# Kernel tuning notes

Hardware: AMD Instinct MI355X
Metric: run time of the kernel (lower is better)

The kernel has to match this reference:

```python
import jax, jax.numpy as jnp
import numpy as np

NUM_POINTS = 1_000_000
WINDOW = 8                      # 2^3 corner stencil for linear shape functions in 3D
GRID = (128, 128, 128)
NUM_CELLS = GRID[0] * GRID[1] * GRID[2]
CELL = 1.0 / 64.0
INV_CELL = 64.0
ORIGIN = jnp.zeros((3,), dtype=jnp.float32)
# forward_window: the 8 corner offsets of the enclosing cell
FWD_WINDOW = jnp.array([[i, j, k] for i in (0, 1) for j in (0, 1) for k in (0, 1)],
                       dtype=jnp.int32)  # [8,3]


def setup_inputs() -> dict:
    key = jax.random.key(0)
    k1, k2, k3 = jax.random.split(key, 3)
    domain = GRID[0] * CELL
    # keep particles one cell away from the boundary so all stencil hashes are in range
    pos = jax.random.uniform(k1, (NUM_POINTS, 3), dtype=jnp.float32) * (domain - 2 * CELL) + CELL
    vel = jax.random.normal(k2, (NUM_POINTS, 3), dtype=jnp.float32)
    mass = jax.random.uniform(k3, (NUM_POINTS,), dtype=jnp.float32) * 1e-3 + 1e-4
    return {"position_stack": pos, "velocity_stack": vel, "mass_stack": mass}


def reference(position_stack, velocity_stack, mass_stack):
    # ---- get_interactions: gather particle pos, hash into grid, shape functions ----
    rel = (position_stack - ORIGIN) * INV_CELL               # [N,3] position in cell units
    base = jnp.floor(rel)                                    # [N,3]
    grid_pos = base[:, None, :] + FWD_WINDOW[None, :, :].astype(rel.dtype)  # [N,8,3]
    dist = rel[:, None, :] - grid_pos                        # [N,8,3], each dim in (-1,1)

    gp = grid_pos.astype(jnp.int32)
    # get_hash, dim==3: pos[2] + pos[0]*grid[2] + pos[1]*grid[2]*grid[0]
    intr_hash = gp[..., 2] + gp[..., 0] * GRID[2] + gp[..., 1] * (GRID[2] * GRID[0])  # [N,8]

    # linear shape function: N = prod_d (1 - |x_d|); grad scaled by inv_cell_size
    w = 1.0 - jnp.abs(dist)                                  # [N,8,3]
    shapef = w[..., 0] * w[..., 1] * w[..., 2]               # [N,8]
    valid = (intr_hash >= 0) & (intr_hash < NUM_CELLS)
    shapef = jnp.where(valid, shapef, 0.0)

    g0 = -jnp.sign(dist[..., 0]) * w[..., 1] * w[..., 2]
    g1 = -jnp.sign(dist[..., 1]) * w[..., 0] * w[..., 2]
    g2 = -jnp.sign(dist[..., 2]) * w[..., 0] * w[..., 1]
    shapef_grad = jnp.stack([g0, g1, g2], axis=-1) * INV_CELL  # [N,8,3]
    shapef_grad = jnp.where(valid[..., None], shapef_grad, 0.0)

    # intr_dist_padded = -dist * cell_size (kept implicitly via dist; used in APIC-style p2g)
    # ---- p2g scatter (vmap_intr_scatter semantics): mass & momentum to grid nodes ----
    h_flat = jnp.clip(intr_hash, 0, NUM_CELLS - 1).reshape(-1)  # [N*8]
    sm = shapef * mass_stack[:, None]                           # [N,8]
    node_mass = jax.ops.segment_sum(sm.reshape(-1), h_flat, num_segments=NUM_CELLS)   # [C]
    mom = sm[..., None] * velocity_stack[:, None, :]            # [N,8,3]
    node_mom = jax.ops.segment_sum(mom.reshape(-1, 3), h_flat, num_segments=NUM_CELLS)  # [C,3]

    return jnp.concatenate([node_mass[:, None], node_mom], axis=1)  # [C,4]
```

## Files before the change

### kernel.cpp

```cpp
#include <hip/hip_runtime.h>
#include <hip/hip_fp16.h>


#define GRID_DIM   128
#define NUM_CELLS  (GRID_DIM * GRID_DIM * GRID_DIM)
#define INV_CELL   64.0f
#define OVF_MAX    65536
#define SCAN_BLKS  2048

#define NREG       512
#define RCAP       2560
#define PPB        2048
#define MAXCAP     3
#define NT2        512
#define NSEG       125
#define NREC       2369
#define EPAD(sc)   ((sc) * 3 + ((sc) >> 2))

typedef float floatx4 __attribute__((ext_vector_type(4)));

__device__ __forceinline__ int cell_id(int ix, int iy, int iz) {
    return iz + ix * GRID_DIM + iy * (GRID_DIM * GRID_DIM);
}

__device__ __forceinline__ unsigned int q16(float f) {
    int q = (int)(f * 65536.0f + 0.5f);
    return (unsigned int)min(q, 65535);
}
__device__ __forceinline__ unsigned int f2h(float f) {
    return (unsigned int)__half_as_ushort(__float2half(f));
}
__device__ __forceinline__ float h2f(unsigned int b) {
    return __half2float(__ushort_as_half((unsigned short)(b & 0xffffu)));
}

__global__ __launch_bounds__(1024) void region_bin_kernel(
    const float* __restrict__ pos, const float* __restrict__ vel,
    const float* __restrict__ mass, unsigned int* __restrict__ region_cursor,
    uint4* __restrict__ regbuf, int* __restrict__ ovf_cnt,
    uint4* __restrict__ ovf_rec, unsigned int* __restrict__ ovf_reg, int n)
{
    __shared__ uint4 rec_lds[PPB];
    __shared__ unsigned short regof[PPB];
    __shared__ unsigned int cnt[NREG];
    __shared__ unsigned int lofs[NREG];
    __shared__ unsigned int gbase[NREG];
    __shared__ unsigned int wtot[8];

    int tid = threadIdx.x;
    int base_i = blockIdx.x * PPB;
    int blockn = min(PPB, n - base_i);

    if (tid < NREG) cnt[tid] = 0;
    __syncthreads();

    uint4 r_[2]; int reg_[2], rank_[2], val_[2];
    #pragma unroll
    for (int k = 0; k < 2; ++k) {
        int e = k * 1024 + tid;
        int i = base_i + e;
        val_[k] = (e < blockn);
        reg_[k] = 0; rank_[k] = 0;
        if (val_[k]) {
            float px = __builtin_nontemporal_load(&pos[3 * i + 0]);
            float py = __builtin_nontemporal_load(&pos[3 * i + 1]);
            float pz = __builtin_nontemporal_load(&pos[3 * i + 2]);
            float rx = px * INV_CELL, ry = py * INV_CELL, rz = pz * INV_CELL;
            float bx = floorf(rx), by = floorf(ry), bz = floorf(rz);
            float fx = rx - bx, fy = ry - by, fz = rz - bz;
            int ix = min(max((int)bx, 0), GRID_DIM - 1);
            int iy = min(max((int)by, 0), GRID_DIM - 1);
            int iz = min(max((int)bz, 0), GRID_DIM - 1);
            int reg = (iz >> 4) | ((ix >> 4) << 3) | ((iy >> 4) << 6);
            unsigned int cid = (unsigned int)((iz & 15) | ((ix & 15) << 4)
                                                        | ((iy & 15) << 8));
            float m  = __builtin_nontemporal_load(&mass[i]);
            float vx = __builtin_nontemporal_load(&vel[3 * i + 0]);
            float vy = __builtin_nontemporal_load(&vel[3 * i + 1]);
            float vz = __builtin_nontemporal_load(&vel[3 * i + 2]);
            uint4 r;
            r.x = q16(fx) | (q16(fy) << 16);
            r.y = q16(fz) | (f2h(m) << 16);
            r.z = f2h(vx) | (f2h(vy) << 16);
            r.w = f2h(vz) | (cid << 16);
            r_[k] = r;
            reg_[k] = reg;
            rank_[k] = (int)atomicAdd(&cnt[reg], 1u);
        }
    }
    __syncthreads();

    unsigned int c = 0, v = 0;
    if (tid < NREG) {
        c = cnt[tid];
        v = c;
        #pragma unroll
        for (int d = 1; d < 64; d <<= 1) {
            unsigned int t = __shfl_up(v, d, 64);
            if ((tid & 63) >= d) v += t;
        }
        if ((tid & 63) == 63) wtot[tid >> 6] = v;
    }
    __syncthreads();
    if (tid == 0) {
        unsigned int run = 0;
        #pragma unroll
        for (int w = 0; w < 8; ++w) { unsigned int t = wtot[w]; wtot[w] = run; run += t; }
    }
    __syncthreads();
    if (tid < NREG) {
        lofs[tid] = wtot[tid >> 6] + v - c;
        if (c) gbase[tid] = atomicAdd(&region_cursor[tid], c);
    }
    __syncthreads();

    #pragma unroll
    for (int k = 0; k < 2; ++k) {
        if (val_[k]) {
            int d = (int)lofs[reg_[k]] + rank_[k];
            rec_lds[d] = r_[k];
            regof[d] = (unsigned short)reg_[k];
        }
    }
    __syncthreads();

    for (int e = tid; e < blockn; e += 1024) {
        uint4 rr = rec_lds[e];
        int rg = (int)regof[e];
        unsigned int slot = gbase[rg] + (unsigned int)(e - (int)lofs[rg]);
        if (slot < (unsigned int)RCAP) {
            regbuf[(size_t)rg * RCAP + slot] = rr;
        } else {
            int o = atomicAdd(ovf_cnt, 1);
            if (o < OVF_MAX) { ovf_rec[o] = rr; ovf_reg[o] = (unsigned int)rg; }
        }
    }
}

__global__ __launch_bounds__(1024) void tile_sort_kernel(
    uint4* __restrict__ regbuf, const unsigned int* __restrict__ region_cursor,
    unsigned int* __restrict__ tile_off)
{
    __shared__ uint4 out_lds[RCAP];
    __shared__ unsigned int cnt[NT2];
    __shared__ unsigned int wsum[8];

    int r = blockIdx.x;
    int tid = threadIdx.x;
    int cntR = (int)min(region_cursor[r], (unsigned int)RCAP);

    if (tid < NT2) cnt[tid] = 0;
    __syncthreads();

    uint4 rr_[3]; int t_[3], rk_[3], vl_[3];
    #pragma unroll
    for (int k = 0; k < 3; ++k) {
        int e = k * 1024 + tid;
        vl_[k] = (e < cntR);
        t_[k] = 0; rk_[k] = 0;
        if (vl_[k]) {
            uint4 rr = regbuf[(size_t)r * RCAP + e];
            unsigned int cid = rr.w >> 16;
            int t = (int)(((cid & 15u) >> 1) | ((((cid >> 4) & 15u) >> 1) << 3)
                                             | ((((cid >> 8) & 15u) >> 1) << 6));
            rr_[k] = rr;
            t_[k] = t;
            rk_[k] = (int)atomicAdd(&cnt[t], 1u);
        }
    }
    __syncthreads();

    unsigned int c = 0, v = 0;
    if (tid < NT2) {
        c = cnt[tid];
        v = c;
        #pragma unroll
        for (int d = 1; d < 64; d <<= 1) {
            unsigned int t = __shfl_up(v, d, 64);
            if ((tid & 63) >= d) v += t;
        }
        if ((tid & 63) == 63) wsum[tid >> 6] = v;
    }
    __syncthreads();
    if (tid == 0) {
        unsigned int run = 0;
        #pragma unroll
        for (int w = 0; w < 8; ++w) { unsigned int t = wsum[w]; wsum[w] = run; run += t; }
    }
    __syncthreads();
    if (tid < NT2) cnt[tid] = wsum[tid >> 6] + v - c;
    __syncthreads();

    #pragma unroll
    for (int k = 0; k < 3; ++k)
        if (vl_[k]) out_lds[(int)cnt[t_[k]] + rk_[k]] = rr_[k];
    __syncthreads();

    for (int e = tid; e < cntR; e += 1024)
        regbuf[(size_t)r * RCAP + e] = out_lds[e];
    if (tid < NT2) tile_off[(size_t)r * (NT2 + 1) + tid] = cnt[tid];
    if (tid == 0) tile_off[(size_t)r * (NT2 + 1) + NT2] = (unsigned int)cntR;
}

__global__ __launch_bounds__(512) void tile_gather2_kernel(
    const uint4* __restrict__ regbuf, const unsigned int* __restrict__ tile_off,
    float4* __restrict__ out)
{
    __shared__ float4 recA[NREC];
    __shared__ unsigned int recB[NREC];
    __shared__ unsigned int cnt_s[729];
    __shared__ unsigned int seg_gb[NSEG];
    __shared__ unsigned short seg_reg[NSEG];
    __shared__ unsigned int seg_off[NSEG + 1];
    __shared__ unsigned int wt2[2];
    __shared__ int ovf_n;
    __shared__ short ovf_sc[64];
    __shared__ uint4 ovf_rec[64];

    int tid = threadIdx.x;
    int swz = (blockIdx.x & 7) * 512 + (blockIdx.x >> 3);
    int bz = swz & 15;
    int bx = (swz >> 4) & 15;
    int by = swz >> 8;
    int g0x = bx * 8, g0y = by * 8, g0z = bz * 8;
    int Tz0 = bz * 4 - 1, Tx0 = bx * 4 - 1, Ty0 = by * 4 - 1;

    for (int s2 = tid; s2 < 729; s2 += 512) cnt_s[s2] = 0;
    if (tid == 0) ovf_n = 0;

    unsigned int c = 0, v = 0;
    if (tid < 128) {
        if (tid < NSEG) {
            int ltz = tid % 5, q = tid / 5, ltx = q % 5, lty = q / 5;
            int Tz = Tz0 + ltz, Tx = Tx0 + ltx, Ty = Ty0 + lty;
            unsigned int gb = 0; int reg = 0;
            if ((Tz >= 0) & (Tx >= 0) & (Ty >= 0)) {
                reg = (Tz >> 3) | ((Tx >> 3) << 3) | ((Ty >> 3) << 6);
                int tl = (Tz & 7) | ((Tx & 7) << 3) | ((Ty & 7) << 6);
                unsigned int o0 = tile_off[(size_t)reg * (NT2 + 1) + tl];
                unsigned int o1 = tile_off[(size_t)reg * (NT2 + 1) + tl + 1];
                c = o1 - o0;
                gb = (unsigned int)reg * RCAP + o0;
            }
            seg_reg[tid] = (unsigned short)reg;
            seg_gb[tid] = gb;
        }
        v = c;
        #pragma unroll
        for (int d = 1; d < 64; d <<= 1) {
            unsigned int t = __shfl_up(v, d, 64);
            if ((tid & 63) >= d) v += t;
        }
        if ((tid & 63) == 63) wt2[tid >> 6] = v;
    }
    __syncthreads();
    if (tid < 128) {
        unsigned int base = (tid >= 64) ? wt2[0] : 0u;
        if (tid < NSEG) seg_off[tid] = base + v - c;
        if (tid == NSEG - 1) seg_off[NSEG] = base + v;
    }
    __syncthreads();
    int R = (int)seg_off[NSEG];

    for (int r = tid; r < R; r += 512) {
        int s = 0;
        #pragma unroll
        for (int step = 64; step >= 1; step >>= 1)
            if (s + step <= NSEG && (int)seg_off[s + step] <= r) s += step;
        int j = r - (int)seg_off[s];
        uint4 rec = regbuf[seg_gb[s] + j];
        unsigned int cid = rec.w >> 16;
        int reg = (int)seg_reg[s];
        int cz = (reg & 7) * 16 + (int)(cid & 15u);
        int cx = ((reg >> 3) & 7) * 16 + (int)((cid >> 4) & 15u);
        int cy = ((reg >> 6) & 7) * 16 + (int)((cid >> 8) & 15u);
        int uz = cz - (g0z - 1), ux = cx - (g0x - 1), uy = cy - (g0y - 1);
        if (((unsigned)uz < 9u) & ((unsigned)ux < 9u) & ((unsigned)uy < 9u)) {
            int sc = uy * 81 + ux * 9 + uz;
            unsigned int j2 = atomicAdd(&cnt_s[sc], 1u);
            if (j2 < MAXCAP) {
                int e = EPAD(sc) + (int)j2;
                float fx = (float)(rec.x & 0xffffu) * (1.0f / 65536.0f);
                float fy = (float)(rec.x >> 16)     * (1.0f / 65536.0f);
                float fz = (float)(rec.y & 0xffffu) * (1.0f / 65536.0f);
                recA[e] = make_float4(fx, fy, fz, __uint_as_float(rec.z));
                recB[e] = (rec.y >> 16) | (rec.w << 16);
            } else {
                int o = atomicAdd(&ovf_n, 1);
                if (o < 64) { ovf_sc[o] = (short)sc; ovf_rec[o] = rec; }
            }
        }
    }
    __syncthreads();

    int tz = tid & 7, tx = (tid >> 3) & 7, ty = tid >> 6;
    float a0 = 0.0f, a1 = 0.0f, a2 = 0.0f, a3 = 0.0f;

    #pragma unroll
    for (int dy = 0; dy < 2; ++dy) {
        #pragma unroll
        for (int dx = 0; dx < 2; ++dx) {
            int scb = (ty + dy) * 81 + (tx + dx) * 9 + tz;
            #pragma unroll
            for (int dz = 0; dz < 2; ++dz) {
                int sc = scb + dz;
                int cnt = min((int)cnt_s[sc], MAXCAP);
                int eb = EPAD(sc);
                for (int j = 0; j < cnt; ++j) {
                    float4 A = recA[eb + j];
                    unsigned int B = recB[eb + j];
                    unsigned int w3 = __float_as_uint(A.w);
                    float wx = dx ? (1.0f - A.x) : A.x;
                    float wy = dy ? (1.0f - A.y) : A.y;
                    float wz = dz ? (1.0f - A.z) : A.z;
                    float sm = wx * wy * wz * h2f(B);
                    a0 += sm;
                    a1 += sm * h2f(w3);
                    a2 += sm * h2f(w3 >> 16);
                    a3 += sm * h2f(B >> 16);
                }
            }
        }
    }

    int no = min(ovf_n, 64);
    for (int e2 = 0; e2 < no; ++e2) {
        int sc = (int)ovf_sc[e2];
        int uzv = sc % 9, t2 = sc / 9, uxv = t2 % 9, uyv = t2 / 9;
        int ddz = uzv - tz, ddx = uxv - tx, ddy = uyv - ty;
        if (((unsigned)ddz < 2u) & ((unsigned)ddx < 2u) & ((unsigned)ddy < 2u)) {
            uint4 rec = ovf_rec[e2];
            float fx = (float)(rec.x & 0xffffu) * (1.0f / 65536.0f);
            float fy = (float)(rec.x >> 16)     * (1.0f / 65536.0f);
            float fz = (float)(rec.y & 0xffffu) * (1.0f / 65536.0f);
            float wx = ddx ? (1.0f - fx) : fx;
            float wy = ddy ? (1.0f - fy) : fy;
            float wz = ddz ? (1.0f - fz) : fz;
            float sm = wx * wy * wz * h2f(rec.y >> 16);
            a0 += sm;
            a1 += sm * h2f(rec.z);
            a2 += sm * h2f(rec.z >> 16);
            a3 += sm * h2f(rec.w);
        }
    }

    int id = (g0z + tz) + (g0x + tx) * GRID_DIM
           + (g0y + ty) * (GRID_DIM * GRID_DIM);
    floatx4 vv = { a0, a1, a2, a3 };
    __builtin_nontemporal_store(vv, (floatx4*)&out[id]);
}

__global__ __launch_bounds__(256) void fixup_packed_kernel(
    const int* __restrict__ ovf_cnt, const uint4* __restrict__ ovf_rec,
    const unsigned int* __restrict__ ovf_reg, float* __restrict__ out)
{
    int total = min(*ovf_cnt, OVF_MAX);
    for (int k = blockIdx.x * 256 + threadIdx.x; k < total; k += gridDim.x * 256) {
        uint4 rec = ovf_rec[k];
        unsigned int reg = ovf_reg[k];
        unsigned int cid = (rec.w >> 16) & 4095u;
        int iz = (int)(reg & 7u) * 16 + (int)(cid & 15u);
        int ix = (int)((reg >> 3) & 7u) * 16 + (int)((cid >> 4) & 15u);
        int iy = (int)((reg >> 6) & 7u) * 16 + (int)((cid >> 8) & 15u);
        float fx = (float)(rec.x & 0xffffu) * (1.0f / 65536.0f);
        float fy = (float)(rec.x >> 16)     * (1.0f / 65536.0f);
        float fz = (float)(rec.y & 0xffffu) * (1.0f / 65536.0f);
        float m  = h2f(rec.y >> 16);
        float vx = h2f(rec.z), vy = h2f(rec.z >> 16), vz = h2f(rec.w);
        float wx[2] = { 1.0f - fx, fx }, wy[2] = { 1.0f - fy, fy }, wz[2] = { 1.0f - fz, fz };
        #pragma unroll
        for (int a = 0; a < 2; ++a)
            #pragma unroll
            for (int b = 0; b < 2; ++b)
                #pragma unroll
                for (int c = 0; c < 2; ++c) {
                    int h = cell_id(ix + a, iy + b, iz + c);
                    bool valid = (h >= 0) && (h < NUM_CELLS);
                    int hc = min(max(h, 0), NUM_CELLS - 1);
                    float s = valid ? (wx[a] * wy[b] * wz[c]) : 0.0f;
                    float sm = s * m;
                    float* cell = out + 4 * (size_t)hc;
                    atomicAdd(cell + 0, sm);
                    atomicAdd(cell + 1, sm * vx);
                    atomicAdd(cell + 2, sm * vy);
                    atomicAdd(cell + 3, sm * vz);
                }
    }
}

__global__ __launch_bounds__(256) void s_hist_kernel(
    const float* __restrict__ pos, int* __restrict__ counts, int n)
{
    int i = blockIdx.x * 256 + threadIdx.x;
    if (i >= n) return;
    int ix = min(max((int)floorf(pos[3 * i + 0] * INV_CELL), 0), GRID_DIM - 1);
    int iy = min(max((int)floorf(pos[3 * i + 1] * INV_CELL), 0), GRID_DIM - 1);
    int iz = min(max((int)floorf(pos[3 * i + 2] * INV_CELL), 0), GRID_DIM - 1);
    atomicAdd(&counts[cell_id(ix, iy, iz)], 1);
}

__global__ __launch_bounds__(256) void s_scan_partials_kernel(
    const int* __restrict__ counts, int* __restrict__ partials)
{
    __shared__ int red[256];
    int t = threadIdx.x;
    int4 v = ((const int4*)counts)[blockIdx.x * 256 + t];
    red[t] = v.x + v.y + v.z + v.w;
    __syncthreads();
    for (int off = 128; off > 0; off >>= 1) {
        if (t < off) red[t] += red[t + off];
        __syncthreads();
    }
    if (t == 0) partials[blockIdx.x] = red[0];
}

__global__ __launch_bounds__(1024) void s_scan_tops_kernel(int* __restrict__ partials)
{
    __shared__ int s[1024];
    int t = threadIdx.x;
    int p0 = partials[2 * t], p1 = partials[2 * t + 1];
    int sum = p0 + p1;
    s[t] = sum;
    __syncthreads();
    for (int off = 1; off < 1024; off <<= 1) {
        int x = (t >= off) ? s[t - off] : 0;
        __syncthreads();
        s[t] += x;
        __syncthreads();
    }
    int excl = s[t] - sum;
    partials[2 * t] = excl;
    partials[2 * t + 1] = excl + p0;
}

__global__ __launch_bounds__(256) void s_scan_final_kernel(
    const int* __restrict__ counts, const int* __restrict__ partials,
    int* __restrict__ offsets, int* __restrict__ cursors)
{
    __shared__ int s[256];
    int t = threadIdx.x;
    int g = blockIdx.x * 256 + t;
    int4 v = ((const int4*)counts)[g];
    int sum = v.x + v.y + v.z + v.w;
    s[t] = sum;
    __syncthreads();
    for (int off = 1; off < 256; off <<= 1) {
        int x = (t >= off) ? s[t - off] : 0;
        __syncthreads();
        s[t] += x;
        __syncthreads();
    }
    int run = partials[blockIdx.x] + s[t] - sum;
    int4 o = make_int4(run, run + v.x, run + v.x + v.y, run + v.x + v.y + v.z);
    ((int4*)offsets)[g] = o;
    ((int4*)cursors)[g] = o;
}

__global__ __launch_bounds__(256) void s_binplace_kernel(
    const float* __restrict__ pos, const float* __restrict__ vel,
    const float* __restrict__ mass, int* __restrict__ cursors,
    float4* __restrict__ records, int n)
{
    int i = blockIdx.x * 256 + threadIdx.x;
    if (i >= n) return;
    float rx = pos[3 * i + 0] * INV_CELL;
    float ry = pos[3 * i + 1] * INV_CELL;
    float rz = pos[3 * i + 2] * INV_CELL;
    int ix = min(max((int)floorf(rx), 0), GRID_DIM - 1);
    int iy = min(max((int)floorf(ry), 0), GRID_DIM - 1);
    int iz = min(max((int)floorf(rz), 0), GRID_DIM - 1);
    int slot = atomicAdd(&cursors[cell_id(ix, iy, iz)], 1);
    records[2 * slot + 0] = make_float4(rx, ry, rz, mass[i]);
    records[2 * slot + 1] = make_float4(vel[3 * i + 0], vel[3 * i + 1],
                                        vel[3 * i + 2], 0.0f);
}

__global__ __launch_bounds__(256) void s_node_gather_kernel(
    const float4* __restrict__ records, const int* __restrict__ offsets,
    const int* __restrict__ cursors, float4* __restrict__ out)
{
    int id = blockIdx.x * 256 + threadIdx.x;
    int gz = id & (GRID_DIM - 1);
    int gx = (id >> 7) & (GRID_DIM - 1);
    int gy = id >> 14;
    float fgx = (float)gx, fgy = (float)gy, fgz = (float)gz;
    float a0 = 0.0f, a1 = 0.0f, a2 = 0.0f, a3 = 0.0f;
    int z0 = max(gz - 1, 0), y0 = max(gy - 1, 0), x0 = max(gx - 1, 0);
    for (int cy = y0; cy <= gy; ++cy) {
        for (int cx = x0; cx <= gx; ++cx) {
            int cb = cx * GRID_DIM + cy * (GRID_DIM * GRID_DIM);
            int beg = offsets[cb + z0];
            int end = cursors[cb + gz];
            for (int p = beg; p < end; ++p) {
                float4 r0 = records[2 * p + 0];
                float4 r1 = records[2 * p + 1];
                float w = (1.0f - fabsf(r0.x - fgx)) *
                          (1.0f - fabsf(r0.y - fgy)) *
                          (1.0f - fabsf(r0.z - fgz));
                float sm = w * r0.w;
                a0 += sm; a1 += sm * r1.x; a2 += sm * r1.y; a3 += sm * r1.z;
            }
        }
    }
    out[id] = make_float4(a0, a1, a2, a3);
}

__global__ __launch_bounds__(256) void p2g_scatter_kernel(
    const float* __restrict__ pos, const float* __restrict__ vel,
    const float* __restrict__ mass, float* __restrict__ out, int n)
{
    int i = blockIdx.x * blockDim.x + threadIdx.x;
    if (i >= n) return;
    float px = pos[3 * i + 0] * INV_CELL;
    float py = pos[3 * i + 1] * INV_CELL;
    float pz = pos[3 * i + 2] * INV_CELL;
    float bx = floorf(px), by = floorf(py), bz = floorf(pz);
    float fx = px - bx, fy = py - by, fz = pz - bz;
    int ix = (int)bx, iy = (int)by, iz = (int)bz;
    float m = mass[i];
    float vx = vel[3 * i + 0], vy = vel[3 * i + 1], vz = vel[3 * i + 2];
    float wx[2] = { 1.0f - fx, fx }, wy[2] = { 1.0f - fy, fy }, wz[2] = { 1.0f - fz, fz };
    #pragma unroll
    for (int a = 0; a < 2; ++a)
        #pragma unroll
        for (int b = 0; b < 2; ++b)
            #pragma unroll
            for (int c = 0; c < 2; ++c) {
                int h = cell_id(ix + a, iy + b, iz + c);
                bool valid = (h >= 0) && (h < NUM_CELLS);
                int hc = min(max(h, 0), NUM_CELLS - 1);
                float s = valid ? (wx[a] * wy[b] * wz[c]) : 0.0f;
                float sm = s * m;
                float* cell = out + 4 * (size_t)hc;
                atomicAdd(cell + 0, sm);
                atomicAdd(cell + 1, sm * vx);
                atomicAdd(cell + 2, sm * vy);
                atomicAdd(cell + 3, sm * vz);
            }
}

extern "C" void kernel_launch(void* const* d_in, const int* in_sizes, int n_in,
                              void* d_out, int out_size, void* d_ws, size_t ws_size,
                              hipStream_t stream) {
    const float* pos  = (const float*)d_in[0];
    const float* vel  = (const float*)d_in[1];
    const float* mass = (const float*)d_in[2];
    float* out = (float*)d_out;
    int n = in_sizes[2];
    int blocks = (n + 255) / 256;

    size_t w_off_tileoff = 4096;
    size_t w_off_ovfcnt  = w_off_tileoff + (size_t)NREG * (NT2 + 1) * 4;
    size_t w_off_ovfrec  = w_off_ovfcnt + 256;
    size_t w_off_ovfreg  = w_off_ovfrec + (size_t)OVF_MAX * 16;
    size_t w_off_regbuf  = w_off_ovfreg + (size_t)OVF_MAX * 4;
    size_t need_twopass  = w_off_regbuf + (size_t)NREG * RCAP * 16;

    size_t s_off_offsets  = (size_t)NUM_CELLS * 4;
    size_t s_off_records  = s_off_offsets + (size_t)NUM_CELLS * 4;
    size_t s_off_partials = s_off_records + (size_t)n * 32;
    size_t need_sorted    = s_off_partials + (size_t)SCAN_BLKS * 4;

    if (ws_size >= need_twopass) {
        char* ws = (char*)d_ws;
        unsigned int* region_cursor = (unsigned int*)ws;
        unsigned int* tile_off = (unsigned int*)(ws + w_off_tileoff);
        int* ovf_cnt           = (int*)(ws + w_off_ovfcnt);
        uint4* ovf_rec         = (uint4*)(ws + w_off_ovfrec);
        unsigned int* ovf_reg  = (unsigned int*)(ws + w_off_ovfreg);
        uint4* regbuf          = (uint4*)(ws + w_off_regbuf);

        (void)hipMemsetAsync(region_cursor, 0, (size_t)NREG * 4, stream);
        (void)hipMemsetAsync(ovf_cnt, 0, 4, stream);
        region_bin_kernel<<<(n + PPB - 1) / PPB, 1024, 0, stream>>>(
            pos, vel, mass, region_cursor, regbuf, ovf_cnt, ovf_rec, ovf_reg, n);
        tile_sort_kernel<<<NREG, 1024, 0, stream>>>(regbuf, region_cursor,
                                                    tile_off);
        tile_gather2_kernel<<<4096, 512, 0, stream>>>(regbuf, tile_off,
                                                      (float4*)out);
        fixup_packed_kernel<<<16, 256, 0, stream>>>(ovf_cnt, ovf_rec,
                                                    ovf_reg, out);
    } else if (ws_size >= need_sorted) {
        char* ws = (char*)d_ws;
        int* counts   = (int*)ws;
        int* offsets  = (int*)(ws + s_off_offsets);
        float4* records = (float4*)(ws + s_off_records);
        int* partials = (int*)(ws + s_off_partials);

        (void)hipMemsetAsync(counts, 0, (size_t)NUM_CELLS * 4, stream);
        s_hist_kernel<<<blocks, 256, 0, stream>>>(pos, counts, n);
        s_scan_partials_kernel<<<SCAN_BLKS, 256, 0, stream>>>(counts, partials);
        s_scan_tops_kernel<<<1, 1024, 0, stream>>>(partials);
        s_scan_final_kernel<<<SCAN_BLKS, 256, 0, stream>>>(counts, partials,
                                                           offsets, counts);
        s_binplace_kernel<<<blocks, 256, 0, stream>>>(pos, vel, mass, counts,
                                                      records, n);
        s_node_gather_kernel<<<NUM_CELLS / 256, 256, 0, stream>>>(
            records, offsets, counts, (float4*)out);
    } else {
        (void)hipMemsetAsync(out, 0, (size_t)out_size * sizeof(float), stream);
        p2g_scatter_kernel<<<blocks, 256, 0, stream>>>(pos, vel, mass, out, n);
    }
}
```

Before: 153.2 us.

## Replace LDS record staging and gather with direct LDS float atomic scatter

The per-block gather kernel no longer stages particle records into capped per-cell LDS slots with an overflow list and then gathers them per node. Each loaded record now scatters its 8 corner contributions directly into a 4x512 LDS accumulator using float atomicAdd. This removes the cell-count atomics, the record buffers, the overflow path and the second gather pass, and lowers LDS use so occupancy can rise. In exchange it issues up to 32 LDS float atomics per record, which may contend on shared nodes, and the summation order becomes nondeterministic.

Result: slower. 304.9 us (+99.0%).

```diff
diff --git a/kernel.cpp b/kernel.cpp
--- a/kernel.cpp
+++ b/kernel.cpp
@@ -11,11 +11,8 @@
 #define NREG       512
 #define RCAP       2560
 #define PPB        2048
-#define MAXCAP     3
 #define NT2        512
 #define NSEG       125
-#define NREC       2369
-#define EPAD(sc)   ((sc) * 3 + ((sc) >> 2))
 
 typedef float floatx4 __attribute__((ext_vector_type(4)));
 
@@ -202,20 +199,15 @@
     if (tid == 0) tile_off[(size_t)r * (NT2 + 1) + NT2] = (unsigned int)cntR;
 }
 
-__global__ __launch_bounds__(512) void tile_gather2_kernel(
+__global__ __launch_bounds__(512) void tile_scatter_gather_kernel(
     const uint4* __restrict__ regbuf, const unsigned int* __restrict__ tile_off,
     float4* __restrict__ out)
 {
-    __shared__ float4 recA[NREC];
-    __shared__ unsigned int recB[NREC];
-    __shared__ unsigned int cnt_s[729];
+    __shared__ float nacc[4 * 512];
     __shared__ unsigned int seg_gb[NSEG];
     __shared__ unsigned short seg_reg[NSEG];
     __shared__ unsigned int seg_off[NSEG + 1];
     __shared__ unsigned int wt2[2];
-    __shared__ int ovf_n;
-    __shared__ short ovf_sc[64];
-    __shared__ uint4 ovf_rec[64];
 
     int tid = threadIdx.x;
     int swz = (blockIdx.x & 7) * 512 + (blockIdx.x >> 3);
@@ -225,8 +217,8 @@
     int g0x = bx * 8, g0y = by * 8, g0z = bz * 8;
     int Tz0 = bz * 4 - 1, Tx0 = bx * 4 - 1, Ty0 = by * 4 - 1;
 
-    for (int s2 = tid; s2 < 729; s2 += 512) cnt_s[s2] = 0;
-    if (tid == 0) ovf_n = 0;
+    nacc[tid] = 0.0f; nacc[512 + tid] = 0.0f;
+    nacc[1024 + tid] = 0.0f; nacc[1536 + tid] = 0.0f;
 
     unsigned int c = 0, v = 0;
     if (tid < 128) {
@@ -274,79 +266,39 @@
         int cz = (reg & 7) * 16 + (int)(cid & 15u);
         int cx = ((reg >> 3) & 7) * 16 + (int)((cid >> 4) & 15u);
         int cy = ((reg >> 6) & 7) * 16 + (int)((cid >> 8) & 15u);
-        int uz = cz - (g0z - 1), ux = cx - (g0x - 1), uy = cy - (g0y - 1);
-        if (((unsigned)uz < 9u) & ((unsigned)ux < 9u) & ((unsigned)uy < 9u)) {
-            int sc = uy * 81 + ux * 9 + uz;
-            unsigned int j2 = atomicAdd(&cnt_s[sc], 1u);
-            if (j2 < MAXCAP) {
-                int e = EPAD(sc) + (int)j2;
-                float fx = (float)(rec.x & 0xffffu) * (1.0f / 65536.0f);
-                float fy = (float)(rec.x >> 16)     * (1.0f / 65536.0f);
-                float fz = (float)(rec.y & 0xffffu) * (1.0f / 65536.0f);
-                recA[e] = make_float4(fx, fy, fz, __uint_as_float(rec.z));
-                recB[e] = (rec.y >> 16) | (rec.w << 16);
-            } else {
-                int o = atomicAdd(&ovf_n, 1);
-                if (o < 64) { ovf_sc[o] = (short)sc; ovf_rec[o] = rec; }
+        float fx = (float)(rec.x & 0xffffu) * (1.0f / 65536.0f);
+        float fy = (float)(rec.x >> 16)     * (1.0f / 65536.0f);
+        float fz = (float)(rec.y & 0xffffu) * (1.0f / 65536.0f);
+        float m  = h2f(rec.y >> 16);
+        float vx = h2f(rec.z), vy = h2f(rec.z >> 16), vz = h2f(rec.w);
+        int lz0 = cz - g0z, lx0 = cx - g0x, ly0 = cy - g0y;
+        #pragma unroll
+        for (int oy = 0; oy < 2; ++oy)
+        #pragma unroll
+        for (int ox = 0; ox < 2; ++ox)
+        #pragma unroll
+        for (int oz = 0; oz < 2; ++oz) {
+            int lz = lz0 + oz, lx = lx0 + ox, ly = ly0 + oy;
+            if (((unsigned)lz < 8u) & ((unsigned)lx < 8u) & ((unsigned)ly < 8u)) {
+                float w = (ox ? fx : 1.0f - fx) *
+                          (oy ? fy : 1.0f - fy) *
+                          (oz ? fz : 1.0f - fz);
+                float sm = w * m;
+                int idx = ly * 64 + lx * 8 + lz;
+                atomicAdd(&nacc[idx], sm);
+                atomicAdd(&nacc[512 + idx], sm * vx);
+                atomicAdd(&nacc[1024 + idx], sm * vy);
+                atomicAdd(&nacc[1536 + idx], sm * vz);
             }
         }
     }
     __syncthreads();
 
     int tz = tid & 7, tx = (tid >> 3) & 7, ty = tid >> 6;
-    float a0 = 0.0f, a1 = 0.0f, a2 = 0.0f, a3 = 0.0f;
-
-    #pragma unroll
-    for (int dy = 0; dy < 2; ++dy) {
-        #pragma unroll
-        for (int dx = 0; dx < 2; ++dx) {
-            int scb = (ty + dy) * 81 + (tx + dx) * 9 + tz;
-            #pragma unroll
-            for (int dz = 0; dz < 2; ++dz) {
-                int sc = scb + dz;
-                int cnt = min((int)cnt_s[sc], MAXCAP);
-                int eb = EPAD(sc);
-                for (int j = 0; j < cnt; ++j) {
-                    float4 A = recA[eb + j];
-                    unsigned int B = recB[eb + j];
-                    unsigned int w3 = __float_as_uint(A.w);
-                    float wx = dx ? (1.0f - A.x) : A.x;
-                    float wy = dy ? (1.0f - A.y) : A.y;
-                    float wz = dz ? (1.0f - A.z) : A.z;
-                    float sm = wx * wy * wz * h2f(B);
-                    a0 += sm;
-                    a1 += sm * h2f(w3);
-                    a2 += sm * h2f(w3 >> 16);
-                    a3 += sm * h2f(B >> 16);
-                }
-            }
-        }
-    }
-
-    int no = min(ovf_n, 64);
-    for (int e2 = 0; e2 < no; ++e2) {
-        int sc = (int)ovf_sc[e2];
-        int uzv = sc % 9, t2 = sc / 9, uxv = t2 % 9, uyv = t2 / 9;
-        int ddz = uzv - tz, ddx = uxv - tx, ddy = uyv - ty;
-        if (((unsigned)ddz < 2u) & ((unsigned)ddx < 2u) & ((unsigned)ddy < 2u)) {
-            uint4 rec = ovf_rec[e2];
-            float fx = (float)(rec.x & 0xffffu) * (1.0f / 65536.0f);
-            float fy = (float)(rec.x >> 16)     * (1.0f / 65536.0f);
-            float fz = (float)(rec.y & 0xffffu) * (1.0f / 65536.0f);
-            float wx = ddx ? (1.0f - fx) : fx;
-            float wy = ddy ? (1.0f - fy) : fy;
-            float wz = ddz ? (1.0f - fz) : fz;
-            float sm = wx * wy * wz * h2f(rec.y >> 16);
-            a0 += sm;
-            a1 += sm * h2f(rec.z);
-            a2 += sm * h2f(rec.z >> 16);
-            a3 += sm * h2f(rec.w);
-        }
-    }
-
     int id = (g0z + tz) + (g0x + tx) * GRID_DIM
            + (g0y + ty) * (GRID_DIM * GRID_DIM);
-    floatx4 vv = { a0, a1, a2, a3 };
+    floatx4 vv = { nacc[tid], nacc[512 + tid], nacc[1024 + tid],
+                   nacc[1536 + tid] };
     __builtin_nontemporal_store(vv, (floatx4*)&out[id]);
 }
 
@@ -576,8 +528,8 @@
             pos, vel, mass, region_cursor, regbuf, ovf_cnt, ovf_rec, ovf_reg, n);
         tile_sort_kernel<<<NREG, 1024, 0, stream>>>(regbuf, region_cursor,
                                                     tile_off);
-        tile_gather2_kernel<<<4096, 512, 0, stream>>>(regbuf, tile_off,
-                                                      (float4*)out);
+        tile_scatter_gather_kernel<<<4096, 512, 0, stream>>>(
+            regbuf, tile_off, (float4*)out);
         fixup_packed_kernel<<<16, 256, 0, stream>>>(ovf_cnt, ovf_rec,
                                                     ovf_reg, out);
     } else if (ws_size >= need_sorted) {
```
